# Optimization experiments

Hardware: AMD Instinct MI355X
Metric: run time of the kernel (lower is better)

## Reference

```python
import jax, jax.numpy as jnp
import numpy as np

B, T, F = 16, 2048, 512


def setup_inputs() -> dict:
    key = jax.random.key(0)
    k1, k2, k3 = jax.random.split(key, 3)
    x = jax.random.normal(k1, (B, T, F), dtype=jnp.float32)
    w_aggr = jax.random.normal(k2, (F, 1), dtype=jnp.float32) * 0.02
    b_aggr = jnp.zeros((1,), dtype=jnp.float32)
    # lengths in [T//2, T] to avoid degenerate lengths[0]==0 (torch would div by 0 too)
    seq_len = jax.random.randint(k3, (B,), T // 2, T + 1).astype(jnp.int32)
    return {"x": x, "w_aggr": w_aggr, "b_aggr": b_aggr, "seq_len": seq_len}


def reference(x, w_aggr, b_aggr, seq_len):
    """Valley-detection dynamic segment-mean pooling.

    Faithful to the torch code, but the O(T^2) triangular-mask bmm is
    expressed as the mathematically identical prefix-sum difference:
    bmm(utri[end]-utri[start], v) == cumsum(v)[end] - cumsum(v)[start].
    Output time dim is padded to T (>= dynamic max_counts); padded segment
    rows have start==end==0 -> numerator 0 / clamp -> exactly 0, matching
    the torch zero-padded `valleys` rows.
    """
    Bx, Tx, Fx = x.shape
    wt = jax.nn.sigmoid(x @ w_aggr + b_aggr)[..., 0]          # [B,T] gate weights
    before = jnp.pad(wt[:, :-1], ((0, 0), (1, 0)))            # pad 0 (sigmoid>0 => pos 0 never valley)
    after = jnp.pad(wt[:, 1:], ((0, 0), (0, 1)))              # pad 0 => pos T-1 never valley
    valley = (wt < before) & (wt < after)                     # [B,T] strict local minima
    starts_mask = valley.at[:, 0].set(True)                   # mask[:,0]=True
    ends_mask = valley.at[:, 0].set(False).at[:, -1].set(True)  # mask[:,0]=False; mask[:,-1]=True

    t = jnp.arange(Tx, dtype=jnp.int32)
    bi = jnp.arange(Bx)[:, None]

    def pack(m, vals):
        # left-pack values at True positions into fixed [B,T] (zeros beyond count)
        rank = jnp.cumsum(m, axis=1) - 1
        slot = jnp.where(m, rank, Tx)                         # dump non-selected into slot T
        out = jnp.zeros((Bx, Tx + 1), jnp.int32).at[bi, slot].set(vals)
        return out[:, :Tx], jnp.sum(m, axis=1)

    starts, counts = pack(starts_mask, jnp.broadcast_to(t, (Bx, Tx)))
    end_vals = jnp.broadcast_to(jnp.minimum(t + 2, Tx), (Bx, Tx))  # valley_index_end clipped to length
    ends, _ = pack(ends_mask, end_vals)

    alpha_h = wt[..., None] * x                               # [B,T,F]
    # exclusive->inclusive prefix sums with leading zero row
    cs_ah = jnp.concatenate([jnp.zeros((Bx, 1, Fx), x.dtype), jnp.cumsum(alpha_h, axis=1)], axis=1)
    cs_w = jnp.concatenate([jnp.zeros((Bx, 1), x.dtype), jnp.cumsum(wt, axis=1)], axis=1)

    num = cs_ah[bi, ends] - cs_ah[bi, starts]                 # [B,T,F] segment sums of w*x
    den = jnp.clip(cs_w[bi, ends] - cs_w[bi, starts], 1e-6, None)[..., None]
    pooled = num / den                                        # weighted segment mean

    max_counts = jnp.max(counts)
    lengths = jnp.minimum(seq_len, Tx)
    new_lengths = (lengths.astype(jnp.float32) / lengths[0].astype(jnp.float32)
                   * max_counts.astype(jnp.float32)).astype(jnp.int32)
    new_mask = t[None, :] < new_lengths[:, None]              # [B,T]
    return pooled, new_mask
```

## Files before the change

kernel.cpp:

```cpp
#include <hip/hip_runtime.h>
#include <math.h>

#define BB 16
#define TT 2048
#define FF 512

#define ACTIVE_BLOCKS 4096
#define ZERO_BLOCKS   1024
#define MASK_BLOCKS   32

typedef float v4f __attribute__((ext_vector_type(4)));

__global__ __launch_bounds__(256) void wt_kernel(const float* __restrict__ x,
                                                 const float* __restrict__ w,
                                                 const float* __restrict__ bias,
                                                 float* __restrict__ wt) {
    int gid  = blockIdx.x * 256 + threadIdx.x;
    int row  = gid >> 6;
    int lane = gid & 63;
    const float* xr = x + (size_t)row * FF + lane * 8;
    const float* wr = w + lane * 8;
    float4 a0 = *(const float4*)xr;
    float4 a1 = *(const float4*)(xr + 4);
    float4 w0 = *(const float4*)wr;
    float4 w1 = *(const float4*)(wr + 4);
    float s = a0.x * w0.x + a0.y * w0.y + a0.z * w0.z + a0.w * w0.w
            + a1.x * w1.x + a1.y * w1.y + a1.z * w1.z + a1.w * w1.w;
#pragma unroll
    for (int off = 32; off > 0; off >>= 1) s += __shfl_xor(s, off, 64);
    if (lane == 0) {
        float z = s + bias[0];
        wt[row] = 1.0f / (1.0f + expf(-z));
    }
}

__global__ __launch_bounds__(64) void seg_kernel(const float* __restrict__ wt,
                                                 int* __restrict__ starts,
                                                 int* __restrict__ ends,
                                                 int* __restrict__ counts) {
    int b    = blockIdx.x;
    int lane = threadIdx.x;
    const float* wrow = wt + b * TT;
    float v[32];
    const float4* p = (const float4*)(wrow + lane * 32);
#pragma unroll
    for (int k = 0; k < 8; ++k) {
        float4 f = p[k];
        v[4*k] = f.x; v[4*k+1] = f.y; v[4*k+2] = f.z; v[4*k+3] = f.w;
    }
    float left  = __shfl_up(v[31], 1, 64);
    float right = __shfl_down(v[0], 1, 64);
    unsigned int flags = 0;
#pragma unroll
    for (int k = 0; k < 32; ++k) {
        int t = lane * 32 + k;
        float prev = (k == 0)  ? left  : v[k - 1];
        float next = (k == 31) ? right : v[k + 1];
        bool val = (t > 0) && (t < TT - 1) && (v[k] < prev) && (v[k] < next);
        if (val) flags |= (1u << k);
    }
    int cnt = __popc(flags);
    int inc = cnt;
#pragma unroll
    for (int off = 1; off < 64; off <<= 1) {
        int y = __shfl_up(inc, off, 64);
        if (lane >= off) inc += y;
    }
    int total = __shfl(inc, 63, 64);
    int r = inc - cnt;
    int* sb = starts + b * TT;
    int* eb = ends + b * TT;
    unsigned int f = flags;
    while (f) {
        int k = __ffs(f) - 1;
        f &= f - 1;
        int t = lane * 32 + k;
        sb[r + 1] = t;
        eb[r] = t + 2;
        ++r;
    }
    if (lane == 0) {
        sb[0] = 0;
        eb[total] = TT;
        counts[b] = total + 1;
    }
}

__global__ __launch_bounds__(256) void pool_kernel(const float* __restrict__ x,
                                                   const float* __restrict__ wt,
                                                   const int* __restrict__ starts,
                                                   const int* __restrict__ ends,
                                                   const int* __restrict__ counts,
                                                   const int* __restrict__ seq_len,
                                                   float* __restrict__ out,
                                                   float* __restrict__ mask_out) {
    int blk = blockIdx.x;
    int tid = threadIdx.x;
    v4f zero = (v4f)(0.f);

    if (blk >= ACTIVE_BLOCKS + ZERO_BLOCKS) {
        int idx = (blk - ACTIVE_BLOCKS - ZERO_BLOCKS) * 256 + tid;
        int maxc = 0;
#pragma unroll
        for (int i = 0; i < BB; ++i) maxc = max(maxc, counts[i]);
        float len0 = (float)min(seq_len[0], TT);
#pragma unroll
        for (int r = 0; r < 4; ++r) {
            int i = idx + r * 8192;
            int b = i >> 11, t = i & (TT - 1);
            int nl = (int)((float)min(seq_len[b], TT) / len0 * (float)maxc);
            mask_out[i] = (t < nl) ? 1.0f : 0.0f;
        }
        return;
    }

    if (blk >= ACTIVE_BLOCKS) {
        int zb = blk - ACTIVE_BLOCKS;
        int b  = zb >> 6;
        int j0 = 1024 + (zb & 63) * 16;
        float* base = out + ((size_t)(b * TT + j0) * FF);
        v4f* dst = (v4f*)base + tid * 2;
        __builtin_nontemporal_store(zero, dst);
        __builtin_nontemporal_store(zero, dst + 1);
        return;
    }

    int b    = blk >> 8;
    int wv   = tid >> 6;
    int lane = tid & 63;
    int j    = (blk & 255) * 4 + wv;
    int row  = b * TT + j;
    float* orow = out + (size_t)row * FF + lane * 8;

    v4f acc0 = (v4f)(0.f);
    v4f acc1 = (v4f)(0.f);
    if (j < counts[b]) {
        int s = __builtin_amdgcn_readfirstlane(starts[row]);
        int e = __builtin_amdgcn_readfirstlane(ends[row]);
        const float* xb   = x + (size_t)b * TT * FF + lane * 8;
        const float* wrow = wt + b * TT;
        float den = 0.f;
        for (int t = s; t < e; t += 4) {
            int i1 = (t + 1 < e) ? t + 1 : t;
            int i2 = (t + 2 < e) ? t + 2 : t;
            int i3 = (t + 3 < e) ? t + 3 : t;
            float w0 = wrow[t];
            float w1 = (t + 1 < e) ? wrow[i1] : 0.f;
            float w2 = (t + 2 < e) ? wrow[i2] : 0.f;
            float w3 = (t + 3 < e) ? wrow[i3] : 0.f;
            const v4f* p0 = (const v4f*)(xb + (size_t)t  * FF);
            const v4f* p1 = (const v4f*)(xb + (size_t)i1 * FF);
            const v4f* p2 = (const v4f*)(xb + (size_t)i2 * FF);
            const v4f* p3 = (const v4f*)(xb + (size_t)i3 * FF);
            v4f v00 = p0[0], v01 = p0[1];
            v4f v10 = p1[0], v11 = p1[1];
            v4f v20 = p2[0], v21 = p2[1];
            v4f v30 = p3[0], v31 = p3[1];
            acc0 += w0 * v00; acc1 += w0 * v01;
            acc0 += w1 * v10; acc1 += w1 * v11;
            acc0 += w2 * v20; acc1 += w2 * v21;
            acc0 += w3 * v30; acc1 += w3 * v31;
            den += w0 + w1 + w2 + w3;
        }
        float inv = 1.0f / fmaxf(den, 1e-6f);
        acc0 *= inv; acc1 *= inv;
    }
    __builtin_nontemporal_store(acc0, (v4f*)orow);
    __builtin_nontemporal_store(acc1, (v4f*)(orow + 4));
}

extern "C" void kernel_launch(void* const* d_in, const int* in_sizes, int n_in,
                              void* d_out, int out_size, void* d_ws, size_t ws_size,
                              hipStream_t stream) {
    const float* x       = (const float*)d_in[0];
    const float* w_aggr  = (const float*)d_in[1];
    const float* b_aggr  = (const float*)d_in[2];
    const int*   seq_len = (const int*)d_in[3];

    float* pooled = (float*)d_out;
    float* mask   = (float*)d_out + (size_t)BB * TT * FF;

    float* wt    = (float*)d_ws;
    int* starts  = (int*)((char*)d_ws + (size_t)BB * TT * 4);
    int* ends    = starts + BB * TT;
    int* counts  = ends + BB * TT;

    wt_kernel<<<(BB * TT) / 4, 256, 0, stream>>>(x, w_aggr, b_aggr, wt);
    seg_kernel<<<BB, 64, 0, stream>>>(wt, starts, ends, counts);
    pool_kernel<<<ACTIVE_BLOCKS + ZERO_BLOCKS + MASK_BLOCKS, 256, 0, stream>>>(
        x, wt, starts, ends, counts, seq_len, pooled, mask);
}
```

Baseline: 125.5 us.

## Pool two adjacent segments per wavefront sharing overlapping x rows

New measurement: 130.3 us. 1.04x slower.

```diff
diff --git a/kernel.cpp b/kernel.cpp
--- a/kernel.cpp
+++ b/kernel.cpp
@@ -5,9 +5,9 @@
 #define TT 2048
 #define FF 512
 
-#define ACTIVE_BLOCKS 4096
-#define ZERO_BLOCKS   1024
-#define MASK_BLOCKS   32
+#define PAIR_BLOCKS 2048
+#define ZERO_BLOCKS 1024
+#define MASK_BLOCKS 32
 
 typedef float v4f __attribute__((ext_vector_type(4)));
 
@@ -98,8 +98,8 @@
     int tid = threadIdx.x;
     v4f zero = (v4f)(0.f);
 
-    if (blk >= ACTIVE_BLOCKS + ZERO_BLOCKS) {
-        int idx = (blk - ACTIVE_BLOCKS - ZERO_BLOCKS) * 256 + tid;
+    if (blk >= PAIR_BLOCKS + ZERO_BLOCKS) {
+        int idx = (blk - PAIR_BLOCKS - ZERO_BLOCKS) * 256 + tid;
         int maxc = 0;
 #pragma unroll
         for (int i = 0; i < BB; ++i) maxc = max(maxc, counts[i]);
@@ -114,8 +114,8 @@
         return;
     }
 
-    if (blk >= ACTIVE_BLOCKS) {
-        int zb = blk - ACTIVE_BLOCKS;
+    if (blk >= PAIR_BLOCKS) {
+        int zb = blk - PAIR_BLOCKS;
         int b  = zb >> 6;
         int j0 = 1024 + (zb & 63) * 16;
         float* base = out + ((size_t)(b * TT + j0) * FF);
@@ -125,48 +125,53 @@
         return;
     }
 
-    int b    = blk >> 8;
+    int b    = blk >> 7;
     int wv   = tid >> 6;
     int lane = tid & 63;
-    int j    = (blk & 255) * 4 + wv;
-    int row  = b * TT + j;
-    float* orow = out + (size_t)row * FF + lane * 8;
+    int p    = (blk & 127) * 4 + wv;
+    int jA   = p * 2;
+    int jB   = jA + 1;
+    int rowA = b * TT + jA;
+    float* orowA = out + (size_t)rowA * FF + lane * 8;
+    float* orowB = orowA + FF;
 
-    v4f acc0 = (v4f)(0.f);
-    v4f acc1 = (v4f)(0.f);
-    if (j < counts[b]) {
-        int s = __builtin_amdgcn_readfirstlane(starts[row]);
-        int e = __builtin_amdgcn_readfirstlane(ends[row]);
+    int cb = counts[b];
+    v4f accA0 = (v4f)(0.f), accA1 = (v4f)(0.f);
+    v4f accB0 = (v4f)(0.f), accB1 = (v4f)(0.f);
+    if (jA < cb) {
+        bool hasB = (jB < cb);
+        int sA = __builtin_amdgcn_readfirstlane(starts[rowA]);
+        int eA = __builtin_amdgcn_readfirstlane(ends[rowA]);
+        int sB = hasB ? __builtin_amdgcn_readfirstlane(starts[rowA + 1]) : eA;
+        int eU = hasB ? __builtin_amdgcn_readfirstlane(ends[rowA + 1]) : eA;
         const float* xb   = x + (size_t)b * TT * FF + lane * 8;
         const float* wrow = wt + b * TT;
-        float den = 0.f;
-        for (int t = s; t < e; t += 4) {
-            int i1 = (t + 1 < e) ? t + 1 : t;
-            int i2 = (t + 2 < e) ? t + 2 : t;
-            int i3 = (t + 3 < e) ? t + 3 : t;
-            float w0 = wrow[t];
-            float w1 = (t + 1 < e) ? wrow[i1] : 0.f;
-            float w2 = (t + 2 < e) ? wrow[i2] : 0.f;
-            float w3 = (t + 3 < e) ? wrow[i3] : 0.f;
-            const v4f* p0 = (const v4f*)(xb + (size_t)t  * FF);
-            const v4f* p1 = (const v4f*)(xb + (size_t)i1 * FF);
-            const v4f* p2 = (const v4f*)(xb + (size_t)i2 * FF);
-            const v4f* p3 = (const v4f*)(xb + (size_t)i3 * FF);
-            v4f v00 = p0[0], v01 = p0[1];
-            v4f v10 = p1[0], v11 = p1[1];
-            v4f v20 = p2[0], v21 = p2[1];
-            v4f v30 = p3[0], v31 = p3[1];
-            acc0 += w0 * v00; acc1 += w0 * v01;
-            acc0 += w1 * v10; acc1 += w1 * v11;
-            acc0 += w2 * v20; acc1 += w2 * v21;
-            acc0 += w3 * v30; acc1 += w3 * v31;
-            den += w0 + w1 + w2 + w3;
+        float denA = 0.f, denB = 0.f;
+        for (int t = sA; t < eU; t += 4) {
+#pragma unroll
+            for (int k = 0; k < 4; ++k) {
+                int tt = t + k;
+                bool in = (tt < eU);
+                int  ti = in ? tt : sA;
+                float wraw = wrow[ti];
+                float wA = (in && tt < eA)  ? wraw : 0.f;
+                float wB = (in && tt >= sB) ? wraw : 0.f;
+                const v4f* pp = (const v4f*)(xb + (size_t)ti * FF);
+                v4f v0 = pp[0], v1 = pp[1];
+                accA0 += wA * v0; accA1 += wA * v1;
+                accB0 += wB * v0; accB1 += wB * v1;
+                denA += wA; denB += wB;
+            }
         }
-        float inv = 1.0f / fmaxf(den, 1e-6f);
-        acc0 *= inv; acc1 *= inv;
+        float invA = 1.0f / fmaxf(denA, 1e-6f);
+        float invB = 1.0f / fmaxf(denB, 1e-6f);
+        accA0 *= invA; accA1 *= invA;
+        accB0 *= invB; accB1 *= invB;
     }
-    __builtin_nontemporal_store(acc0, (v4f*)orow);
-    __builtin_nontemporal_store(acc1, (v4f*)(orow + 4));
+    __builtin_nontemporal_store(accA0, (v4f*)orowA);
+    __builtin_nontemporal_store(accA1, (v4f*)(orowA + 4));
+    __builtin_nontemporal_store(accB0, (v4f*)orowB);
+    __builtin_nontemporal_store(accB1, (v4f*)(orowB + 4));
 }
 
 extern "C" void kernel_launch(void* const* d_in, const int* in_sizes, int n_in,
@@ -187,6 +192,6 @@
 
     wt_kernel<<<(BB * TT) / 4, 256, 0, stream>>>(x, w_aggr, b_aggr, wt);
     seg_kernel<<<BB, 64, 0, stream>>>(wt, starts, ends, counts);
-    pool_kernel<<<ACTIVE_BLOCKS + ZERO_BLOCKS + MASK_BLOCKS, 256, 0, stream>>>(
+    pool_kernel<<<PAIR_BLOCKS + ZERO_BLOCKS + MASK_BLOCKS, 256, 0, stream>>>(
         x, wt, starts, ends, counts, seq_len, pooled, mask);
 }
```

## Split each pooled row across two wavefronts and unroll segment loop by eight

Applied to the files above, without the earlier changes.

After: 129.4 us. 1.03x slower.

```diff
diff --git a/kernel.cpp b/kernel.cpp
--- a/kernel.cpp
+++ b/kernel.cpp
@@ -5,7 +5,7 @@
 #define TT 2048
 #define FF 512
 
-#define ACTIVE_BLOCKS 4096
+#define ACTIVE_BLOCKS 8192
 #define ZERO_BLOCKS   1024
 #define MASK_BLOCKS   32
 
@@ -125,48 +125,45 @@
         return;
     }
 
-    int b    = blk >> 8;
-    int wv   = tid >> 6;
-    int lane = tid & 63;
-    int j    = (blk & 255) * 4 + wv;
-    int row  = b * TT + j;
-    float* orow = out + (size_t)row * FF + lane * 8;
+    int wv    = tid >> 6;
+    int lane  = tid & 63;
+    int aw    = blk * 4 + wv;
+    int rowid = aw >> 1;
+    int half  = aw & 1;
+    int b     = rowid >> 10;
+    int j     = rowid & 1023;
+    int row   = b * TT + j;
+    int fo    = half * 256 + lane * 4;
 
-    v4f acc0 = (v4f)(0.f);
-    v4f acc1 = (v4f)(0.f);
+    v4f acc = (v4f)(0.f);
     if (j < counts[b]) {
         int s = __builtin_amdgcn_readfirstlane(starts[row]);
         int e = __builtin_amdgcn_readfirstlane(ends[row]);
-        const float* xb   = x + (size_t)b * TT * FF + lane * 8;
+        const float* xb   = x + (size_t)b * TT * FF + fo;
         const float* wrow = wt + b * TT;
         float den = 0.f;
-        for (int t = s; t < e; t += 4) {
-            int i1 = (t + 1 < e) ? t + 1 : t;
-            int i2 = (t + 2 < e) ? t + 2 : t;
-            int i3 = (t + 3 < e) ? t + 3 : t;
-            float w0 = wrow[t];
-            float w1 = (t + 1 < e) ? wrow[i1] : 0.f;
-            float w2 = (t + 2 < e) ? wrow[i2] : 0.f;
-            float w3 = (t + 3 < e) ? wrow[i3] : 0.f;
-            const v4f* p0 = (const v4f*)(xb + (size_t)t  * FF);
-            const v4f* p1 = (const v4f*)(xb + (size_t)i1 * FF);
-            const v4f* p2 = (const v4f*)(xb + (size_t)i2 * FF);
-            const v4f* p3 = (const v4f*)(xb + (size_t)i3 * FF);
-            v4f v00 = p0[0], v01 = p0[1];
-            v4f v10 = p1[0], v11 = p1[1];
-            v4f v20 = p2[0], v21 = p2[1];
-            v4f v30 = p3[0], v31 = p3[1];
-            acc0 += w0 * v00; acc1 += w0 * v01;
-            acc0 += w1 * v10; acc1 += w1 * v11;
-            acc0 += w2 * v20; acc1 += w2 * v21;
-            acc0 += w3 * v30; acc1 += w3 * v31;
-            den += w0 + w1 + w2 + w3;
+        for (int t = s; t < e; t += 8) {
+            int   ii[8];
+            float ww[8];
+#pragma unroll
+            for (int k = 0; k < 8; ++k) {
+                int tt = t + k;
+                bool in = (tt < e);
+                ii[k] = in ? tt : t;
+                ww[k] = in ? wrow[ii[k]] : 0.f;
+            }
+#pragma unroll
+            for (int k = 0; k < 8; ++k) {
+                const v4f* p = (const v4f*)(xb + (size_t)ii[k] * FF);
+                v4f v0 = p[0];
+                acc += ww[k] * v0;
+                den += ww[k];
+            }
         }
-        float inv = 1.0f / fmaxf(den, 1e-6f);
-        acc0 *= inv; acc1 *= inv;
+        acc *= 1.0f / fmaxf(den, 1e-6f);
     }
-    __builtin_nontemporal_store(acc0, (v4f*)orow);
-    __builtin_nontemporal_store(acc1, (v4f*)(orow + 4));
+    float* orow = out + (size_t)row * FF + fo;
+    __builtin_nontemporal_store(acc, (v4f*)orow);
 }
 
 extern "C" void kernel_launch(void* const* d_in, const int* in_sizes, int n_in,
```
